# Optimization experiments

Hardware: AMD Instinct MI355X
Metric: run time of the kernel (lower is better)

Reference implementation:

```python
import jax, jax.numpy as jnp
import numpy as np

RADIUS = 0.1
NSAMPLE = 32
STRIDE = 4
EPS = 1e-5


def fps(p, M):
    # Furthest point sampling. p: [B, N, 3] -> idx [B, M] int32. First point is index 0.
    B, N, _ = p.shape

    def body(carry, _):
        dmin, last = carry
        lp = jnp.take_along_axis(p, last[:, None, None], axis=1)  # [B,1,3]
        d = jnp.sum((p - lp) ** 2, axis=-1)                       # [B,N]
        dmin = jnp.minimum(dmin, d)
        nxt = jnp.argmax(dmin, axis=-1).astype(jnp.int32)
        return (dmin, nxt), nxt

    first = jnp.zeros((B,), jnp.int32)
    dmin0 = jnp.full((B, N), jnp.inf, p.dtype)
    _, rest = jax.lax.scan(body, (dmin0, first), None, length=M - 1)
    return jnp.concatenate([first[None, :], rest], axis=0).T  # [B,M]


def ball_query(new_p, p, radius, K):
    # For each query, first K support indices with dist < radius (CUDA ballquery semantics:
    # pad with first found index; 0 if none). new_p [B,M,3], p [B,N,3] -> [B,M,K] int32.
    N = p.shape[1]
    d2 = (jnp.sum(new_p ** 2, -1)[:, :, None] + jnp.sum(p ** 2, -1)[:, None, :]
          - 2.0 * jnp.einsum('bmd,bnd->bmn', new_p, p))  # [B,M,N]
    scores = jnp.where(d2 < radius * radius,
                       jnp.arange(N, dtype=jnp.int32)[None, None, :], N)
    neg_vals, _ = jax.lax.top_k(-scores, K)  # K smallest scores, ascending
    idx = -neg_vals
    first = jnp.where(idx[..., :1] >= N, 0, idx[..., :1])
    return jnp.where(idx >= N, first, idx)


def bn(x, g, b):
    # BatchNorm (training-mode batch stats) over all dims except channel dim 1.
    axes = tuple(i for i in range(x.ndim) if i != 1)
    m = jnp.mean(x, axes, keepdims=True)
    v = jnp.var(x, axes, keepdims=True)
    shape = (1, -1) + (1,) * (x.ndim - 2)
    return g.reshape(shape) * (x - m) * jax.lax.rsqrt(v + EPS) + b.reshape(shape)


def setup_inputs() -> dict:
    key = jax.random.key(0)
    ks = jax.random.split(key, 6)
    B, N, C = 4, 8192, 64
    return {
        'p': jax.random.uniform(ks[0], (B, N, 3), jnp.float32),
        'f': jax.random.normal(ks[1], (B, C, N), jnp.float32),
        'w1': jax.random.normal(ks[2], (64, 3 + C), jnp.float32) * 0.05,
        'g1': jnp.ones((64,), jnp.float32),
        'b1': jnp.zeros((64,), jnp.float32),
        'w2': jax.random.normal(ks[3], (128, 64), jnp.float32) * 0.05,
        'g2': jnp.ones((128,), jnp.float32),
        'b2': jnp.zeros((128,), jnp.float32),
        'w_skip': jax.random.normal(ks[4], (128, C), jnp.float32) * 0.05,
        'b_skip': jnp.zeros((128,), jnp.float32),
    }


def reference(p, f, w1, g1, b1, w2, g2, b2, w_skip, b_skip):
    B, N, _ = p.shape
    C = f.shape[1]
    M = N // STRIDE
    idx = fps(p, M)                                                # [B,M]
    new_p = jnp.take_along_axis(p, idx[:, :, None], axis=1)        # [B,M,3]
    # residual branch: gather sampled features, 1x1 conv1d skip
    fi = jnp.take_along_axis(f, jnp.broadcast_to(idx[:, None, :], (B, C, M)), axis=2)
    identity = jnp.einsum('oc,bcm->bom', w_skip, fi) + b_skip[None, :, None]
    # ball-query grouping
    nidx = ball_query(new_p, p, RADIUS, NSAMPLE)                   # [B,M,K]
    flat = nidx.reshape(B, 1, M * NSAMPLE)
    pj = jnp.take_along_axis(p.transpose(0, 2, 1),
                             jnp.broadcast_to(flat, (B, 3, M * NSAMPLE)),
                             axis=2).reshape(B, 3, M, NSAMPLE)
    dp = pj - new_p.transpose(0, 2, 1)[:, :, :, None]              # [B,3,M,K]
    fj = jnp.take_along_axis(f, jnp.broadcast_to(flat, (B, C, M * NSAMPLE)),
                             axis=2).reshape(B, C, M, NSAMPLE)
    x = jnp.concatenate([dp, fj], axis=1)                          # [B,3+C,M,K]
    # conv-bn-relu, conv-bn (last block no act because use_res)
    x = jax.nn.relu(bn(jnp.einsum('oc,bcmk->bomk', w1, x), g1, b1))
    x = bn(jnp.einsum('oc,bcmk->bomk', w2, x), g2, b2)
    fout = jnp.max(x, axis=-1)                                     # [B,128,M]
    fout = jax.nn.relu(fout + identity)
    return new_p, fout, idx
```

## Files before the change

kernel.cpp:

```cpp
#include <hip/hip_runtime.h>
#include <math.h>

#define BB 4
#define NP 8192
#define CF 64
#define MQ 2048
#define KS 32

#define WS_FT     0u
#define WS_NIDX   2097152u
#define WS_IDXI   2359296u
#define WS_ST1    2367488u
#define WS_ST2    2375680u
#define WS_SC1    2392064u
#define WS_SC2    2392192u
#define WS_MAXY2  2392448u
#define WS_W1P    3441024u

typedef float v2f __attribute__((ext_vector_type(2)));

__global__ __launch_bounds__(256) void transpose_f_kernel(
    const float* __restrict__ f, float* __restrict__ ft) {
  __shared__ float tile[64][65];
  int b = blockIdx.y;
  int n0 = blockIdx.x * 64;
  int cc = threadIdx.x >> 6;
  int nn = threadIdx.x & 63;
  #pragma unroll
  for (int r = 0; r < 16; ++r) {
    int c = cc * 16 + r;
    tile[c][nn] = f[((size_t)b * 64 + c) * NP + n0 + nn];
  }
  __syncthreads();
  #pragma unroll
  for (int r = 0; r < 16; ++r) {
    int nl = cc * 16 + r;
    ft[((size_t)b * NP + n0 + nl) * 64 + nn] = tile[nn][nl];
  }
}

__global__ void prep_w1_kernel(const float* __restrict__ w1, float* __restrict__ w1p) {
  int i = blockIdx.x * 256 + threadIdx.x;
  if (i < 64 * 68) {
    int o = i / 68, c = i % 68;
    w1p[i] = (c < 67) ? w1[o * 67 + c] : 0.0f;
  }
}

#define FPS_T 256
#define PPT 32

template <int CTRL>
__device__ __forceinline__ unsigned long long dpp_max_step(unsigned long long k) {
  int lo = (int)(unsigned)k;
  int hi = (int)(unsigned)(k >> 32);
  int slo = __builtin_amdgcn_update_dpp(0, lo, CTRL, 0xF, 0xF, true);
  int shi = __builtin_amdgcn_update_dpp(0, hi, CTRL, 0xF, 0xF, true);
  unsigned long long s =
      ((unsigned long long)(unsigned)shi << 32) | (unsigned long long)(unsigned)slo;
  return s > k ? s : k;
}

__global__ __launch_bounds__(256, 1) void fps_kernel(
    const float* __restrict__ p, float* __restrict__ out, int* __restrict__ idx_i) {
#pragma clang fp contract(off)
  __shared__ float4 sp4[NP];
  __shared__ int win[MQ];
  __shared__ __align__(16) unsigned long long wkey[2][4];
  int b = blockIdx.x;
  const float* pb = p + (size_t)b * NP * 3;
  float* out_newp = out;
  float* out_idxf = out + BB*MQ*3 + (size_t)BB*128*MQ;
  int t = threadIdx.x;

  v2f px2[16], py2[16], pz2[16], dmin2[16];
  #pragma unroll
  for (int k = 0; k < 16; ++k) {
    int i0 = (2*k) * FPS_T + t;
    int i1 = i0 + FPS_T;
    float x0 = pb[i0*3+0], y0 = pb[i0*3+1], z0 = pb[i0*3+2];
    float x1 = pb[i1*3+0], y1 = pb[i1*3+1], z1 = pb[i1*3+2];
    px2[k] = (v2f){x0, x1}; py2[k] = (v2f){y0, y1}; pz2[k] = (v2f){z0, z1};
    sp4[i0] = make_float4(x0, y0, z0, 0.0f);
    sp4[i1] = make_float4(x1, y1, z1, 0.0f);
    dmin2[k] = (v2f){INFINITY, INFINITY};
  }
  if (t == 0) win[0] = 0;
  __syncthreads();
  float lx = sp4[0].x, ly = sp4[0].y, lz = sp4[0].z;
  unsigned nt = ~(unsigned)t;

  for (int j = 1; j < MQ; ++j) {
#pragma clang fp contract(off)
    v2f l2x = (v2f){lx, lx}, l2y = (v2f){ly, ly}, l2z = (v2f){lz, lz};
    float bv0 = -1.0f, bv1 = -1.0f;
    unsigned bn0 = 0u, bn1 = 0u;
    #pragma unroll
    for (int k = 0; k < 16; ++k) {
      v2f dx = px2[k] - l2x;
      v2f dy = py2[k] - l2y;
      v2f dz = pz2[k] - l2z;
      v2f dd = ((dx*dx) + (dy*dy)) + (dz*dz);
      v2f dm = __builtin_elementwise_min(dmin2[k], dd);
      dmin2[k] = dm;
      float m0 = dm.x, m1 = dm.y;
      bool g0 = m0 > bv0;
      bv0 = g0 ? m0 : bv0;
      bn0 = g0 ? (nt - (unsigned)((2*k) * FPS_T)) : bn0;
      bool g1 = m1 > bv1;
      bv1 = g1 ? m1 : bv1;
      bn1 = g1 ? (nt - (unsigned)((2*k+1) * FPS_T)) : bn1;
    }
    unsigned long long k0 =
        ((unsigned long long)__float_as_uint(bv0) << 32) | (unsigned long long)bn0;
    unsigned long long k1 =
        ((unsigned long long)__float_as_uint(bv1) << 32) | (unsigned long long)bn1;
    unsigned long long key = k0 > k1 ? k0 : k1;
    key = dpp_max_step<0x111>(key);
    key = dpp_max_step<0x112>(key);
    key = dpp_max_step<0x114>(key);
    key = dpp_max_step<0x118>(key);
    key = dpp_max_step<0x142>(key);
    key = dpp_max_step<0x143>(key);
    if ((t & 63) == 63) wkey[j & 1][t >> 6] = key;
    __syncthreads();
    const ulonglong2* wk2 = (const ulonglong2*)(&wkey[j & 1][0]);
    ulonglong2 ka = wk2[0];
    ulonglong2 kb = wk2[1];
    unsigned long long m0 = ka.x > ka.y ? ka.x : ka.y;
    unsigned long long m1 = kb.x > kb.y ? kb.x : kb.y;
    unsigned long long kw = m0 > m1 ? m0 : m1;
    int wi = (int)(~(unsigned)kw);
    float4 c = sp4[wi];
    lx = c.x; ly = c.y; lz = c.z;
    if (t == 0) win[j] = wi;
  }

  __syncthreads();
  #pragma unroll
  for (int k = 0; k < MQ / FPS_T; ++k) {
    int j = k * FPS_T + t;
    int wi = win[j];
    out_idxf[b*MQ + j] = (float)wi;
    idx_i[b*MQ + j] = wi;
    float4 c = sp4[wi];
    float* np_ = &out_newp[(size_t)(b*MQ + j) * 3];
    np_[0] = c.x; np_[1] = c.y; np_[2] = c.z;
  }
}

__global__ __launch_bounds__(256) void ballq_kernel(
    const float* __restrict__ p, const float* __restrict__ newp,
    int* __restrict__ nidx) {
  int qid = blockIdx.x * 4 + (threadIdx.x >> 6);
  int lane = threadIdx.x & 63;
  int b = qid >> 11;
  const float* pb = p + (size_t)b * NP * 3;
  float qx = newp[qid*3], qy = newp[qid*3+1], qz = newp[qid*3+2];
  float sq_q = __fadd_rn(__fadd_rn(__fmul_rn(qx,qx), __fmul_rn(qy,qy)), __fmul_rn(qz,qz));
  const float R2 = (float)(0.1 * 0.1);
  int found = 0, first = -1;
  int* outp = nidx + (size_t)qid * KS;
  for (int base = 0; base < NP; base += 64) {
    int n = base + lane;
    float x = pb[n*3], y = pb[n*3+1], z = pb[n*3+2];
    float sq_p = __fadd_rn(__fadd_rn(__fmul_rn(x,x), __fmul_rn(y,y)), __fmul_rn(z,z));
    float dot  = __fadd_rn(__fadd_rn(__fmul_rn(qx,x), __fmul_rn(qy,y)), __fmul_rn(qz,z));
    float d2   = __fadd_rn(__fadd_rn(sq_q, sq_p), __fmul_rn(-2.0f, dot));
    bool hit = d2 < R2;
    unsigned long long mask = __ballot(hit);
    if (mask) {
      if (first < 0) first = base + __builtin_ctzll(mask);
      int cnt = __popcll(mask);
      if (found < KS) {
        int rank = __popcll(mask & ((1ull << lane) - 1ull));
        if (hit && found + rank < KS) outp[found + rank] = n;
      }
      found += cnt;
      if (found >= KS) break;
    }
  }
  int fcl = found < KS ? found : KS;
  int padv = first < 0 ? 0 : first;
  if (lane >= fcl && lane < KS) outp[lane] = padv;
}

__global__ __launch_bounds__(256) void p1_kernel(
    const float* __restrict__ p, const float* __restrict__ newp,
    const float* __restrict__ ft, const int* __restrict__ nidx,
    const float* __restrict__ w1p, float* __restrict__ stats1) {
  __shared__ __align__(16) float xbuf[4][KS][68];
  __shared__ float wbs[4][64], wbq[4][64];
  int wv = threadIdx.x >> 6, lane = threadIdx.x & 63;
  int qid = blockIdx.x * 4 + wv;
  int b = qid >> 11;
  int nv = (lane < KS) ? nidx[(size_t)qid * KS + lane] : 0;
  float qx = newp[qid*3], qy = newp[qid*3+1], qz = newp[qid*3+2];
  for (int kk = 0; kk < KS; ++kk) {
    int n = __shfl(nv, kk);
    const float* fr = ft + ((size_t)b * NP + n) * 64;
    xbuf[wv][kk][3 + lane] = fr[lane];
    if (lane < 3) {
      const float* pp = p + ((size_t)b * NP + n) * 3;
      float qc = (lane == 0) ? qx : ((lane == 1) ? qy : qz);
      xbuf[wv][kk][lane] = __fsub_rn(pp[lane], qc);
    }
    if (lane == 3) xbuf[wv][kk][67] = 0.0f;
  }
  __syncthreads();
  const float4* wr = (const float4*)(w1p + lane * 68);
  float4 wreg[17];
  #pragma unroll
  for (int c4 = 0; c4 < 17; ++c4) wreg[c4] = wr[c4];
  float ss = 0.f, qq = 0.f;
  for (int kk = 0; kk < KS; ++kk) {
    const float4* xr = (const float4*)(&xbuf[wv][kk][0]);
    float acc = 0.f;
    #pragma unroll
    for (int c4 = 0; c4 < 17; ++c4) {
      float4 w = wreg[c4]; float4 x = xr[c4];
      acc += w.x*x.x + w.y*x.y + w.z*x.z + w.w*x.w;
    }
    ss += acc; qq += acc * acc;
  }
  wbs[wv][lane] = ss; wbq[wv][lane] = qq;
  __syncthreads();
  if (threadIdx.x < 64) {
    float s  = wbs[0][threadIdx.x] + wbs[1][threadIdx.x] + wbs[2][threadIdx.x] + wbs[3][threadIdx.x];
    float s2 = wbq[0][threadIdx.x] + wbq[1][threadIdx.x] + wbq[2][threadIdx.x] + wbq[3][threadIdx.x];
    int slice = blockIdx.x & 63;
    atomicAdd(&stats1[(slice*2+0)*64 + threadIdx.x], s);
    atomicAdd(&stats1[(slice*2+1)*64 + threadIdx.x], s2);
  }
}

__global__ void fin1_kernel(const float* __restrict__ stats1,
                            const float* __restrict__ g, const float* __restrict__ bb,
                            float* __restrict__ sc) {
  int o = threadIdx.x;
  float s = 0.f, q = 0.f;
  for (int sl = 0; sl < 64; ++sl) { s += stats1[(sl*2+0)*64+o]; q += stats1[(sl*2+1)*64+o]; }
  const float cnt = (float)(BB * MQ * KS);
  float mean = s / cnt;
  float var = q / cnt - mean * mean;
  float rstd = 1.0f / sqrtf(var + 1e-5f);
  float gs = g[o] * rstd;
  sc[o] = gs;
  sc[64+o] = bb[o] - mean * gs;
}

__global__ void fin2_kernel(const float* __restrict__ stats2,
                            const float* __restrict__ g, const float* __restrict__ bb,
                            float* __restrict__ sc) {
  int o = threadIdx.x;
  float s = 0.f, q = 0.f;
  for (int sl = 0; sl < 64; ++sl) { s += stats2[(sl*2+0)*128+o]; q += stats2[(sl*2+1)*128+o]; }
  const float cnt = (float)(BB * MQ * KS);
  float mean = s / cnt;
  float var = q / cnt - mean * mean;
  float rstd = 1.0f / sqrtf(var + 1e-5f);
  float gs = g[o] * rstd;
  sc[o] = gs;
  sc[128+o] = bb[o] - mean * gs;
}

__global__ __launch_bounds__(256) void p2_kernel(
    const float* __restrict__ p, const float* __restrict__ newp,
    const float* __restrict__ ft, const int* __restrict__ nidx,
    const float* __restrict__ w1p, const float* __restrict__ w2,
    const float* __restrict__ sc1,
    float* __restrict__ stats2, float* __restrict__ maxy2) {
  __shared__ __align__(16) float xbuf[4][KS][68];
  __shared__ float wbs[4][128], wbq[4][128];
  int wv = threadIdx.x >> 6, lane = threadIdx.x & 63;
  int qid = blockIdx.x * 4 + wv;
  int b = qid >> 11;
  int nv = (lane < KS) ? nidx[(size_t)qid * KS + lane] : 0;
  float qx = newp[qid*3], qy = newp[qid*3+1], qz = newp[qid*3+2];
  for (int kk = 0; kk < KS; ++kk) {
    int n = __shfl(nv, kk);
    const float* fr = ft + ((size_t)b * NP + n) * 64;
    xbuf[wv][kk][3 + lane] = fr[lane];
    if (lane < 3) {
      const float* pp = p + ((size_t)b * NP + n) * 3;
      float qc = (lane == 0) ? qx : ((lane == 1) ? qy : qz);
      xbuf[wv][kk][lane] = __fsub_rn(pp[lane], qc);
    }
    if (lane == 3) xbuf[wv][kk][67] = 0.0f;
  }
  __syncthreads();
  {
    const float4* wr = (const float4*)(w1p + lane * 68);
    float4 wreg[17];
    #pragma unroll
    for (int c4 = 0; c4 < 17; ++c4) wreg[c4] = wr[c4];
    float s1v = sc1[lane], t1v = sc1[64 + lane];
    for (int kk = 0; kk < KS; ++kk) {
      const float4* xr = (const float4*)(&xbuf[wv][kk][0]);
      float acc = 0.f;
      #pragma unroll
      for (int c4 = 0; c4 < 17; ++c4) {
        float4 w = wreg[c4]; float4 x = xr[c4];
        acc += w.x*x.x + w.y*x.y + w.z*x.z + w.w*x.w;
      }
      float h = fmaxf(0.0f, fmaf(acc, s1v, t1v));
      xbuf[wv][kk][lane] = h;
    }
  }
  const float4* w2a = (const float4*)(w2 + (size_t)lane * 64);
  const float4* w2b = (const float4*)(w2 + (size_t)(lane + 64) * 64);
  float4 wra[16], wrb[16];
  #pragma unroll
  for (int c4 = 0; c4 < 16; ++c4) { wra[c4] = w2a[c4]; wrb[c4] = w2b[c4]; }
  float ss0 = 0.f, qq0 = 0.f, mx0 = -INFINITY;
  float ss1 = 0.f, qq1 = 0.f, mx1 = -INFINITY;
  for (int kk = 0; kk < KS; ++kk) {
    const float4* hr = (const float4*)(&xbuf[wv][kk][0]);
    float a0 = 0.f, a1 = 0.f;
    #pragma unroll
    for (int c4 = 0; c4 < 16; ++c4) {
      float4 h4 = hr[c4];
      float4 wa = wra[c4]; float4 wb = wrb[c4];
      a0 += wa.x*h4.x + wa.y*h4.y + wa.z*h4.z + wa.w*h4.w;
      a1 += wb.x*h4.x + wb.y*h4.y + wb.z*h4.z + wb.w*h4.w;
    }
    ss0 += a0; qq0 += a0*a0; mx0 = fmaxf(mx0, a0);
    ss1 += a1; qq1 += a1*a1; mx1 = fmaxf(mx1, a1);
  }
  maxy2[(size_t)qid * 128 + lane] = mx0;
  maxy2[(size_t)qid * 128 + 64 + lane] = mx1;
  wbs[wv][lane] = ss0; wbs[wv][64+lane] = ss1;
  wbq[wv][lane] = qq0; wbq[wv][64+lane] = qq1;
  __syncthreads();
  if (threadIdx.x < 128) {
    float s  = wbs[0][threadIdx.x] + wbs[1][threadIdx.x] + wbs[2][threadIdx.x] + wbs[3][threadIdx.x];
    float s2 = wbq[0][threadIdx.x] + wbq[1][threadIdx.x] + wbq[2][threadIdx.x] + wbq[3][threadIdx.x];
    int slice = blockIdx.x & 63;
    atomicAdd(&stats2[(slice*2+0)*128 + threadIdx.x], s);
    atomicAdd(&stats2[(slice*2+1)*128 + threadIdx.x], s2);
  }
}

__global__ __launch_bounds__(256) void p3_kernel(
    const float* __restrict__ ft, const int* __restrict__ idx_i,
    const float* __restrict__ w_skip, const float* __restrict__ b_skip,
    const float* __restrict__ sc2, const float* __restrict__ maxy2,
    float* __restrict__ outf) {
  int wv = threadIdx.x >> 6, lane = threadIdx.x & 63;
  int qid = blockIdx.x * 4 + wv;
  int b = qid >> 11, m = qid & (MQ - 1);
  int n = idx_i[qid];
  const float4* f4 = (const float4*)(ft + ((size_t)b * NP + n) * 64);
  const float4* wa = (const float4*)(w_skip + (size_t)lane * 64);
  const float4* wb = (const float4*)(w_skip + (size_t)(lane + 64) * 64);
  float a0 = b_skip[lane], a1 = b_skip[lane + 64];
  #pragma unroll
  for (int c4 = 0; c4 < 16; ++c4) {
    float4 x = f4[c4]; float4 u = wa[c4]; float4 v = wb[c4];
    a0 += u.x*x.x + u.y*x.y + u.z*x.z + u.w*x.w;
    a1 += v.x*x.x + v.y*x.y + v.z*x.z + v.w*x.w;
  }
  float v0 = maxy2[(size_t)qid * 128 + lane];
  float v1 = maxy2[(size_t)qid * 128 + 64 + lane];
  float r0 = fmaxf(0.0f, fmaf(v0, sc2[lane],      sc2[128 + lane])      + a0);
  float r1 = fmaxf(0.0f, fmaf(v1, sc2[lane + 64], sc2[128 + lane + 64]) + a1);
  outf[((size_t)b * 128 + lane) * MQ + m] = r0;
  outf[((size_t)b * 128 + lane + 64) * MQ + m] = r1;
}

extern "C" void kernel_launch(void* const* d_in, const int* in_sizes, int n_in,
                              void* d_out, int out_size, void* d_ws, size_t ws_size,
                              hipStream_t stream) {
  (void)in_sizes; (void)n_in; (void)out_size; (void)ws_size;
  const float* p   = (const float*)d_in[0];
  const float* f   = (const float*)d_in[1];
  const float* w1  = (const float*)d_in[2];
  const float* g1  = (const float*)d_in[3];
  const float* b1  = (const float*)d_in[4];
  const float* w2  = (const float*)d_in[5];
  const float* g2  = (const float*)d_in[6];
  const float* b2  = (const float*)d_in[7];
  const float* wsk = (const float*)d_in[8];
  const float* bsk = (const float*)d_in[9];
  float* out = (float*)d_out;
  float* wsf = (float*)d_ws;

  float* ft    = wsf + WS_FT;
  int*   nidx  = (int*)(wsf + WS_NIDX);
  int*   idxi  = (int*)(wsf + WS_IDXI);
  float* st1   = wsf + WS_ST1;
  float* st2   = wsf + WS_ST2;
  float* sc1   = wsf + WS_SC1;
  float* sc2   = wsf + WS_SC2;
  float* maxy2 = wsf + WS_MAXY2;
  float* w1p   = wsf + WS_W1P;

  float* out_newp = out;
  float* out_f    = out + BB*MQ*3;

  (void)hipMemsetAsync(st1, 0, (8192 + 16384) * sizeof(float), stream);

  transpose_f_kernel<<<dim3(NP/64, BB), 256, 0, stream>>>(f, ft);
  prep_w1_kernel<<<17, 256, 0, stream>>>(w1, w1p);
  fps_kernel<<<BB, FPS_T, 0, stream>>>(p, out, idxi);
  ballq_kernel<<<BB*MQ/4, 256, 0, stream>>>(p, out_newp, nidx);
  p1_kernel<<<BB*MQ/4, 256, 0, stream>>>(p, out_newp, ft, nidx, w1p, st1);
  fin1_kernel<<<1, 64, 0, stream>>>(st1, g1, b1, sc1);
  p2_kernel<<<BB*MQ/4, 256, 0, stream>>>(p, out_newp, ft, nidx, w1p, w2, sc1, st2, maxy2);
  fin2_kernel<<<1, 128, 0, stream>>>(st2, g2, b2, sc2);
  p3_kernel<<<BB*MQ/4, 256, 0, stream>>>(ft, idxi, wsk, bsk, sc2, maxy2, out_f);
}
```

Measured before the change: 2.069 ms.

## Fuse transpose and weight-prep into FPS launch; track loop index in argmax

The feature transpose and w1 padding kernels are folded into the FPS kernel as extra blocks, so they run alongside the four long-running FPS blocks instead of as separate serial launches. Inside the FPS loop the argmax now records only the unrolled slot index and rebuilds the point index after the loop, which cuts per-iteration integer work. The dmin vectors are split into scalar arrays. The extra blocks share the large static LDS allocation and may compete with the FPS blocks for resources.

```diff
diff --git a/kernel.cpp b/kernel.cpp
--- a/kernel.cpp
+++ b/kernel.cpp
@@ -19,36 +19,8 @@
 
 typedef float v2f __attribute__((ext_vector_type(2)));
 
-__global__ __launch_bounds__(256) void transpose_f_kernel(
-    const float* __restrict__ f, float* __restrict__ ft) {
-  __shared__ float tile[64][65];
-  int b = blockIdx.y;
-  int n0 = blockIdx.x * 64;
-  int cc = threadIdx.x >> 6;
-  int nn = threadIdx.x & 63;
-  #pragma unroll
-  for (int r = 0; r < 16; ++r) {
-    int c = cc * 16 + r;
-    tile[c][nn] = f[((size_t)b * 64 + c) * NP + n0 + nn];
-  }
-  __syncthreads();
-  #pragma unroll
-  for (int r = 0; r < 16; ++r) {
-    int nl = cc * 16 + r;
-    ft[((size_t)b * NP + n0 + nl) * 64 + nn] = tile[nn][nl];
-  }
-}
-
-__global__ void prep_w1_kernel(const float* __restrict__ w1, float* __restrict__ w1p) {
-  int i = blockIdx.x * 256 + threadIdx.x;
-  if (i < 64 * 68) {
-    int o = i / 68, c = i % 68;
-    w1p[i] = (c < 67) ? w1[o * 67 + c] : 0.0f;
-  }
-}
-
 #define FPS_T 256
-#define PPT 32
+#define FPS_NK 16
 
 template <int CTRL>
 __device__ __forceinline__ unsigned long long dpp_max_step(unsigned long long k) {
@@ -61,21 +33,57 @@
   return s > k ? s : k;
 }
 
-__global__ __launch_bounds__(256, 1) void fps_kernel(
-    const float* __restrict__ p, float* __restrict__ out, int* __restrict__ idx_i) {
+__global__ __launch_bounds__(256, 1) void fps_fused_kernel(
+    const float* __restrict__ p, float* __restrict__ out, int* __restrict__ idx_i,
+    const float* __restrict__ f, float* __restrict__ ft,
+    const float* __restrict__ w1, float* __restrict__ w1p) {
 #pragma clang fp contract(off)
-  __shared__ float4 sp4[NP];
-  __shared__ int win[MQ];
-  __shared__ __align__(16) unsigned long long wkey[2][4];
-  int b = blockIdx.x;
+  __shared__ __align__(16) char smem[NP * 16 + MQ * 4 + 2 * 4 * 8];
+  int bx = blockIdx.x;
+  int t = threadIdx.x;
+
+  if (bx >= 4) {
+    if (bx < 4 + 512) {
+      float (*tile)[65] = (float (*)[65])smem;
+      int tb = bx - 4;
+      int b = tb >> 7;
+      int n0 = (tb & 127) * 64;
+      int cc = t >> 6;
+      int nn = t & 63;
+      #pragma unroll
+      for (int r = 0; r < 16; ++r) {
+        int c = cc * 16 + r;
+        tile[c][nn] = f[((size_t)b * 64 + c) * NP + n0 + nn];
+      }
+      __syncthreads();
+      #pragma unroll
+      for (int r = 0; r < 16; ++r) {
+        int nl = cc * 16 + r;
+        ft[((size_t)b * NP + n0 + nl) * 64 + nn] = tile[nn][nl];
+      }
+    } else {
+      int i = (bx - 516) * 256 + t;
+      if (i < 64 * 68) {
+        int o = i / 68, c = i % 68;
+        w1p[i] = (c < 67) ? w1[o * 67 + c] : 0.0f;
+      }
+    }
+    return;
+  }
+
+  float4* sp4 = (float4*)smem;
+  int* win = (int*)(smem + NP * 16);
+  unsigned long long* wkey = (unsigned long long*)(smem + NP * 16 + MQ * 4);
+
+  int b = bx;
   const float* pb = p + (size_t)b * NP * 3;
   float* out_newp = out;
   float* out_idxf = out + BB*MQ*3 + (size_t)BB*128*MQ;
-  int t = threadIdx.x;
-
-  v2f px2[16], py2[16], pz2[16], dmin2[16];
+
+  v2f px2[FPS_NK], py2[FPS_NK], pz2[FPS_NK];
+  float dmn0[FPS_NK], dmn1[FPS_NK];
   #pragma unroll
-  for (int k = 0; k < 16; ++k) {
+  for (int k = 0; k < FPS_NK; ++k) {
     int i0 = (2*k) * FPS_T + t;
     int i1 = i0 + FPS_T;
     float x0 = pb[i0*3+0], y0 = pb[i0*3+1], z0 = pb[i0*3+2];
@@ -83,7 +91,7 @@
     px2[k] = (v2f){x0, x1}; py2[k] = (v2f){y0, y1}; pz2[k] = (v2f){z0, z1};
     sp4[i0] = make_float4(x0, y0, z0, 0.0f);
     sp4[i1] = make_float4(x1, y1, z1, 0.0f);
-    dmin2[k] = (v2f){INFINITY, INFINITY};
+    dmn0[k] = INFINITY; dmn1[k] = INFINITY;
   }
   if (t == 0) win[0] = 0;
   __syncthreads();
@@ -94,23 +102,24 @@
 #pragma clang fp contract(off)
     v2f l2x = (v2f){lx, lx}, l2y = (v2f){ly, ly}, l2z = (v2f){lz, lz};
     float bv0 = -1.0f, bv1 = -1.0f;
-    unsigned bn0 = 0u, bn1 = 0u;
+    unsigned bk0 = 0u, bk1 = 0u;
     #pragma unroll
-    for (int k = 0; k < 16; ++k) {
+    for (int k = 0; k < FPS_NK; ++k) {
       v2f dx = px2[k] - l2x;
       v2f dy = py2[k] - l2y;
       v2f dz = pz2[k] - l2z;
       v2f dd = ((dx*dx) + (dy*dy)) + (dz*dz);
-      v2f dm = __builtin_elementwise_min(dmin2[k], dd);
-      dmin2[k] = dm;
-      float m0 = dm.x, m1 = dm.y;
+      float m0 = fminf(dmn0[k], dd.x);  dmn0[k] = m0;
+      float m1 = fminf(dmn1[k], dd.y);  dmn1[k] = m1;
       bool g0 = m0 > bv0;
       bv0 = g0 ? m0 : bv0;
-      bn0 = g0 ? (nt - (unsigned)((2*k) * FPS_T)) : bn0;
+      bk0 = g0 ? (unsigned)k : bk0;
       bool g1 = m1 > bv1;
       bv1 = g1 ? m1 : bv1;
-      bn1 = g1 ? (nt - (unsigned)((2*k+1) * FPS_T)) : bn1;
-    }
+      bk1 = g1 ? (unsigned)k : bk1;
+    }
+    unsigned bn0 = nt - (bk0 << 9);
+    unsigned bn1 = nt - (bk1 << 9) - 256u;
     unsigned long long k0 =
         ((unsigned long long)__float_as_uint(bv0) << 32) | (unsigned long long)bn0;
     unsigned long long k1 =
@@ -122,9 +131,9 @@
     key = dpp_max_step<0x118>(key);
     key = dpp_max_step<0x142>(key);
     key = dpp_max_step<0x143>(key);
-    if ((t & 63) == 63) wkey[j & 1][t >> 6] = key;
+    if ((t & 63) == 63) wkey[(j & 1) * 4 + (t >> 6)] = key;
     __syncthreads();
-    const ulonglong2* wk2 = (const ulonglong2*)(&wkey[j & 1][0]);
+    const ulonglong2* wk2 = (const ulonglong2*)(&wkey[(j & 1) * 4]);
     ulonglong2 ka = wk2[0];
     ulonglong2 kb = wk2[1];
     unsigned long long m0 = ka.x > ka.y ? ka.x : ka.y;
@@ -400,9 +409,7 @@
 
   (void)hipMemsetAsync(st1, 0, (8192 + 16384) * sizeof(float), stream);
 
-  transpose_f_kernel<<<dim3(NP/64, BB), 256, 0, stream>>>(f, ft);
-  prep_w1_kernel<<<17, 256, 0, stream>>>(w1, w1p);
-  fps_kernel<<<BB, FPS_T, 0, stream>>>(p, out, idxi);
+  fps_fused_kernel<<<4 + 512 + 17, FPS_T, 0, stream>>>(p, out, idxi, f, ft, w1, w1p);
   ballq_kernel<<<BB*MQ/4, 256, 0, stream>>>(p, out_newp, nidx);
   p1_kernel<<<BB*MQ/4, 256, 0, stream>>>(p, out_newp, ft, nidx, w1p, st1);
   fin1_kernel<<<1, 64, 0, stream>>>(st1, g1, b1, sc1);
```

Result: no change. 2.084 ms (+0.7%).
